# Kernel tuning notes

Hardware: AMD Instinct MI355X
Metric: run time of the kernel (lower is better)

## Reference

```python
import jax, jax.numpy as jnp
import numpy as np

MAX_ITER = 3
MIN = -1e32


def setup_inputs() -> dict:
    key = jax.random.key(0)
    k1, k2 = jax.random.split(key)
    B, L = 8, 160
    s_arc = jax.random.normal(k1, (B, L, L), dtype=jnp.float32)
    s_sib = jax.random.normal(k2, (B, L, L, L), dtype=jnp.float32)
    mask = jnp.ones((B, L), dtype=bool)
    return {"s_arc": s_arc, "s_sib": s_sib, "mask": mask}


def _lbp(s_arc, s_sib, mask):
    B, L = mask.shape
    ar = jnp.arange(L)
    ls = jnp.minimum(ar[:, None], ar[None, :])  # [L,L] min(i,j)
    rs = jnp.maximum(ar[:, None], ar[None, :])  # [L,L] max(i,j)
    mask = mask.at[:, 0].set(True)  # root always on
    # pairwise token mask, permuted to [L, L, B]
    m2 = (mask[:, :, None] & mask[:, None, :]).transpose(2, 1, 0)
    # second-order mask [head, dep, sib, B]
    mask2o = m2[:, None, :, :] & m2[:, :, None, :]
    mask2o = mask2o & (ls[:, :, None] != ar[None, None, :])[..., None]
    mask2o = mask2o & (rs[:, :, None] != ar[None, None, :])[..., None]
    s_arc_p = s_arc.transpose(2, 1, 0)  # [head, dep, B]
    s_sib_p = jnp.where(mask2o, s_sib.transpose(2, 1, 3, 0), MIN)  # [head, dep, sib, B]
    q = s_arc_p
    m_sib = jnp.zeros((L, L, L, B), dtype=s_arc.dtype)
    for _ in range(MAX_ITER):
        q = jax.nn.log_softmax(q, axis=0)  # normalize over heads
        m = q[:, :, None, :] - m_sib  # [h, d, s, B]
        m_sib = jax.nn.log_softmax(
            jnp.logaddexp(jax.nn.logsumexp(m, axis=0), m + s_sib_p).transpose(0, 2, 1, 3),
            axis=0,
        )
        q = s_arc_p + jnp.sum(m_sib * mask2o, axis=2)
    return q.transpose(2, 1, 0)  # [B, dep, head]


def reference(s_arc, s_sib, mask):
    logits = _lbp(s_arc, s_sib, mask)
    marginals = jax.nn.softmax(logits, axis=-1)
    return marginals
```

## Files before the change

kernel.cpp:

```cpp
#include <hip/hip_runtime.h>
#include <math.h>


constexpr int L = 160;
constexpr int B = 8;
constexpr int NT = 256;
constexpr int CHUNK = 32;
constexpr float INV_LN2 = 1.4426950408889634f;

#if __has_builtin(__builtin_amdgcn_exp2f)
__device__ __forceinline__ float ex2(float x) { return __builtin_amdgcn_exp2f(x); }
#else
__device__ __forceinline__ float ex2(float x) { return exp2f(x); }
#endif
#if __has_builtin(__builtin_amdgcn_logf)
__device__ __forceinline__ float lg2(float x) { return __builtin_amdgcn_logf(x); }
#else
__device__ __forceinline__ float lg2(float x) { return log2f(x); }
#endif

template <int IMM>
__device__ __forceinline__ float swz(float v) {
  return __int_as_float(__builtin_amdgcn_ds_swizzle(__float_as_int(v), IMM));
}
template <int CTRL>
__device__ __forceinline__ float dppmov(float x) {
  return __int_as_float(
      __builtin_amdgcn_update_dpp(0, __float_as_int(x), CTRL, 0xF, 0xF, true));
}
__device__ __forceinline__ void rsum64x2(float& a, float& b) {
  a += dppmov<0x121>(a); b += dppmov<0x121>(b);
  a += dppmov<0x122>(a); b += dppmov<0x122>(b);
  a += dppmov<0x124>(a); b += dppmov<0x124>(b);
  a += dppmov<0x128>(a); b += dppmov<0x128>(b);
  a += swz<0x401F>(a);   b += swz<0x401F>(b);
  a += __shfl_xor(a, 32, 64);
  b += __shfl_xor(b, 32, 64);
}
__device__ __forceinline__ float wsum(float v) {
  v += swz<0x041F>(v); v += swz<0x081F>(v); v += swz<0x101F>(v);
  v += swz<0x201F>(v); v += swz<0x401F>(v);
  v += __shfl_xor(v, 32, 64);
  return v;
}
__device__ __forceinline__ float wmax(float v) {
  v = fmaxf(v, swz<0x041F>(v)); v = fmaxf(v, swz<0x081F>(v));
  v = fmaxf(v, swz<0x101F>(v)); v = fmaxf(v, swz<0x201F>(v));
  v = fmaxf(v, swz<0x401F>(v));
  v = fmaxf(v, __shfl_xor(v, 32, 64));
  return v;
}

template <bool FIRST>
__device__ __forceinline__ void phaseAB(const float* __restrict__ s_arc,
                                        const float* __restrict__ Min, int slab,
                                        int b, int d, int t, int lane,
                                        float* qn, float4 (*qpart)[40], float* s_lse) {
  if constexpr (!FIRST) {
    if (t < 240) {
      const int h4 = t % 40, sr = t / 40;
      float ax = 0.f, ay = 0.f, az = 0.f, aw = 0.f;
#pragma unroll 4
      for (int i = 0; i < 27; ++i) {
        const int s = sr + 6 * i;
        if (s < L) {
          const float4 v = *reinterpret_cast<const float4*>(Min + slab + s * L + 4 * h4);
          ax += (s != 4 * h4 + 0 && s != d) ? v.x : 0.f;
          ay += (s != 4 * h4 + 1 && s != d) ? v.y : 0.f;
          az += (s != 4 * h4 + 2 && s != d) ? v.z : 0.f;
          aw += (s != 4 * h4 + 3 && s != d) ? v.w : 0.f;
        }
      }
      qpart[sr][h4] = make_float4(ax, ay, az, aw);
    }
    __syncthreads();
    if (t < 40) {
      float4 a = qpart[0][t];
#pragma unroll
      for (int sr = 1; sr < 6; ++sr) {
        const float4 p = qpart[sr][t];
        a.x += p.x; a.y += p.y; a.z += p.z; a.w += p.w;
      }
      const float4 sa = *reinterpret_cast<const float4*>(s_arc + (b * L + d) * L + 4 * t);
      a.x += sa.x * INV_LN2; a.y += sa.y * INV_LN2;
      a.z += sa.z * INV_LN2; a.w += sa.w * INV_LN2;
      *reinterpret_cast<float4*>(qn + 4 * t) = a;
    }
  } else {
    if (t < 40) {
      float4 sa = *reinterpret_cast<const float4*>(s_arc + (b * L + d) * L + 4 * t);
      sa.x *= INV_LN2; sa.y *= INV_LN2; sa.z *= INV_LN2; sa.w *= INV_LN2;
      *reinterpret_cast<float4*>(qn + 4 * t) = sa;
    }
  }
  __syncthreads();
  if (t < 64) {
    const int h0 = lane, h1 = lane + 64, h2 = lane + 128;
    const bool has2 = lane < 32;
    float v0 = qn[h0], v1 = qn[h1];
    float v2 = has2 ? qn[h2] : -INFINITY;
    float mx = wmax(fmaxf(fmaxf(v0, v1), v2));
    float sm = wsum(ex2(v0 - mx) + ex2(v1 - mx) + (has2 ? ex2(v2 - mx) : 0.f));
    if (lane == 0) *s_lse = mx + lg2(sm);
  }
  __syncthreads();
  if (t < L) qn[t] -= *s_lse;
  __syncthreads();
}

template <bool FIRST>
__global__ __launch_bounds__(NT) void lbp_iter(const float* __restrict__ s_arc,
                                               const float* __restrict__ s_sib,
                                               const float* __restrict__ Min,
                                               float* __restrict__ Mout) {
  const int d = blockIdx.x, b = blockIdx.y;
  const int t = threadIdx.x, lane = t & 63, w = t >> 6;

  __shared__ __align__(16) float qn[L];
  __shared__ __align__(16) float4 qpart[6][40];
  __shared__ __align__(16) float ss2[CHUNK][L];
  __shared__ float s_lse;

  const int slab = (b * L + d) * (L * L);

  phaseAB<FIRST>(s_arc, Min, slab, b, d, t, lane, qn, qpart, &s_lse);

  float q0 = 0.f, q1 = 0.f, q2 = 0.f, q3 = 0.f;
  if (lane < 40) {
    const float4 qv = *reinterpret_cast<const float4*>(qn + 4 * lane);
    q0 = qv.x; q1 = qv.y; q2 = qv.z; q3 = qv.w;
  }

  for (int c = 0; c < L / CHUNK; ++c) {
    const int s0 = c * CHUNK;
    const float* base = s_sib + slab;
    float4 sv[5];
#pragma unroll
    for (int i = 0; i < 5; ++i) {
      const int f = t + NT * i;
      const int h = f >> 3, sl4 = f & 7;
      sv[i] = *reinterpret_cast<const float4*>(base + h * L + s0 + 4 * sl4);
    }
    const int sw = s0 + w * 8;
    float4 mr[8];
    if constexpr (!FIRST) {
      if (lane < 40) {
#pragma unroll
        for (int i = 0; i < 8; ++i)
          mr[i] = *reinterpret_cast<const float4*>(Min + slab + (sw + i) * L + 4 * lane);
      }
    }
#pragma unroll
    for (int i = 0; i < 5; ++i) {
      const int f = t + NT * i;
      const int h = f >> 3, sl4 = f & 7;
      const int h4 = h >> 2, e = h & 3;
      const float* vv = reinterpret_cast<const float*>(&sv[i]);
#pragma unroll
      for (int j = 0; j < 4; ++j) {
        const int sl = 4 * sl4 + j;
        const int cc = (sl + (sl >> 3)) & 7;
        ss2[sl][4 * (h4 ^ cc) + e] = vv[j] * INV_LN2;
      }
    }
    __syncthreads();

#pragma unroll
    for (int i = 0; i < 8; ++i) {
      const int s = sw + i;
      const int sl = s - s0;
      float s1 = 0.f, s2 = 0.f, et0 = 0.f, et1 = 0.f, et2 = 0.f, et3 = 0.f;
      if (lane < 40) {
        const int cc = (sl + (sl >> 3)) & 7;
        const float4 ssv = *reinterpret_cast<const float4*>(&ss2[sl][4 * (lane ^ cc)]);
        float mm0, mm1, mm2, mm3;
        if constexpr (FIRST) {
          mm0 = q0; mm1 = q1; mm2 = q2; mm3 = q3;
        } else {
          mm0 = q0 - mr[i].x; mm1 = q1 - mr[i].y;
          mm2 = q2 - mr[i].z; mm3 = q3 - mr[i].w;
        }
        s1 = ex2(mm0) + ex2(mm1) + ex2(mm2) + ex2(mm3);
        const int hb = 4 * lane;
        et0 = (s != hb + 0 && s != d) ? ex2(mm0 + ssv.x) : 0.f;
        et1 = (s != hb + 1 && s != d) ? ex2(mm1 + ssv.y) : 0.f;
        et2 = (s != hb + 2 && s != d) ? ex2(mm2 + ssv.z) : 0.f;
        et3 = (s != hb + 3 && s != d) ? ex2(mm3 + ssv.w) : 0.f;
        s2 = et0 + et1 + et2 + et3;
      }
      rsum64x2(s1, s2);
      if (lane < 40) {
        const float nd = lg2(160.f * s1 + s2);
        float4 o;
        o.x = lg2(s1 + et0) - nd;
        o.y = lg2(s1 + et1) - nd;
        o.z = lg2(s1 + et2) - nd;
        o.w = lg2(s1 + et3) - nd;
        *reinterpret_cast<float4*>(Mout + ((b * L + s) * L + d) * L + 4 * lane) = o;
      }
    }
    __syncthreads();
  }
}

__global__ __launch_bounds__(NT) void lbp_final(const float* __restrict__ s_arc,
                                                const float* __restrict__ Min,
                                                float* __restrict__ out) {
  const int d = blockIdx.x, b = blockIdx.y;
  const int t = threadIdx.x, lane = t & 63;
  __shared__ __align__(16) float qn[L];
  __shared__ __align__(16) float4 qpart[6][40];
  __shared__ float s_lse;
  const int slab = (b * L + d) * (L * L);

  phaseAB<false>(s_arc, Min, slab, b, d, t, lane, qn, qpart, &s_lse);

  if (t < L) out[(b * L + d) * L + t] = ex2(qn[t]);
}

extern "C" void kernel_launch(void* const* d_in, const int* in_sizes, int n_in,
                              void* d_out, int out_size, void* d_ws, size_t ws_size,
                              hipStream_t stream) {
  (void)in_sizes; (void)n_in; (void)out_size; (void)ws_size;
  const float* s_arc = (const float*)d_in[0];
  const float* s_sib = (const float*)d_in[1];
  float* out = (float*)d_out;

  const size_t MELEMS = (size_t)B * L * L * L;
  float* MA = (float*)d_ws;
  float* MB = MA + MELEMS;

  dim3 grid(L, B), block(NT);
  hipLaunchKernelGGL((lbp_iter<true>), grid, block, 0, stream, s_arc, s_sib, (const float*)nullptr, MA);
  hipLaunchKernelGGL((lbp_iter<false>), grid, block, 0, stream, s_arc, s_sib, MA, MB);
  hipLaunchKernelGGL((lbp_iter<false>), grid, block, 0, stream, s_arc, s_sib, MB, MA);
  hipLaunchKernelGGL(lbp_final, grid, block, 0, stream, s_arc, MA, out);
}
```

Baseline: 430.7 us.

## Prefetch next s_sib chunk and batch wave reductions via DPP row scans

Loads the next chunk of s_sib into registers while the current chunk is being computed, and only writes it to shared memory after the compute step. This overlaps global loads with the exp/log work. The per-row wave reductions are batched four at a time using DPP row_shr and row_bcast scans, with lane 63 read back via readlane instead of swizzle and shuffle. In the first iteration it also drops the s1 sum and uses S1 = 1, on the basis that q is normalized. The trade-off is higher register pressure from holding the prefetch buffer and the batched arrays.

```diff
diff --git a/kernel.cpp b/kernel.cpp
--- a/kernel.cpp
+++ b/kernel.cpp
@@ -23,19 +23,34 @@
 __device__ __forceinline__ float swz(float v) {
   return __int_as_float(__builtin_amdgcn_ds_swizzle(__float_as_int(v), IMM));
 }
-template <int CTRL>
-__device__ __forceinline__ float dppmov(float x) {
-  return __int_as_float(
-      __builtin_amdgcn_update_dpp(0, __float_as_int(x), CTRL, 0xF, 0xF, true));
-}
-__device__ __forceinline__ void rsum64x2(float& a, float& b) {
-  a += dppmov<0x121>(a); b += dppmov<0x121>(b);
-  a += dppmov<0x122>(a); b += dppmov<0x122>(b);
-  a += dppmov<0x124>(a); b += dppmov<0x124>(b);
-  a += dppmov<0x128>(a); b += dppmov<0x128>(b);
-  a += swz<0x401F>(a);   b += swz<0x401F>(b);
-  a += __shfl_xor(a, 32, 64);
-  b += __shfl_xor(b, 32, 64);
+template <int CTRL, int RM>
+__device__ __forceinline__ float dppadd(float v) {
+  return v + __int_as_float(__builtin_amdgcn_update_dpp(
+                 0, __float_as_int(v), CTRL, RM, 0xF, true));
+}
+template <int CTRL, int RM>
+__device__ __forceinline__ void dstep2(float (&a)[4], float (&b)[4]) {
+#pragma unroll
+  for (int k = 0; k < 4; ++k) {
+    a[k] = dppadd<CTRL, RM>(a[k]);
+    b[k] = dppadd<CTRL, RM>(b[k]);
+  }
+}
+__device__ __forceinline__ void scanreduce2(float (&a)[4], float (&b)[4]) {
+  dstep2<0x111, 0xF>(a, b); dstep2<0x112, 0xF>(a, b); dstep2<0x114, 0xF>(a, b);
+  dstep2<0x118, 0xF>(a, b); dstep2<0x142, 0xA>(a, b); dstep2<0x143, 0xC>(a, b);
+}
+template <int CTRL, int RM>
+__device__ __forceinline__ void dstep1(float (&b)[4]) {
+#pragma unroll
+  for (int k = 0; k < 4; ++k) b[k] = dppadd<CTRL, RM>(b[k]);
+}
+__device__ __forceinline__ void scanreduce1(float (&b)[4]) {
+  dstep1<0x111, 0xF>(b); dstep1<0x112, 0xF>(b); dstep1<0x114, 0xF>(b);
+  dstep1<0x118, 0xF>(b); dstep1<0x142, 0xA>(b); dstep1<0x143, 0xC>(b);
+}
+__device__ __forceinline__ float bcast63(float v) {
+  return __int_as_float(__builtin_amdgcn_readlane(__float_as_int(v), 63));
 }
 __device__ __forceinline__ float wsum(float v) {
   v += swz<0x041F>(v); v += swz<0x081F>(v); v += swz<0x101F>(v);
@@ -131,15 +146,39 @@
     q0 = qv.x; q1 = qv.y; q2 = qv.z; q3 = qv.w;
   }
 
+  const float* base = s_sib + slab;
+  float4 sv[5];
+  auto stage_write = [&]() {
+#pragma unroll
+    for (int i = 0; i < 5; ++i) {
+      const int f = t + NT * i, h = f >> 3, sl4 = f & 7;
+      const int h4 = h >> 2, e = h & 3;
+      const float* vv = reinterpret_cast<const float*>(&sv[i]);
+#pragma unroll
+      for (int j = 0; j < 4; ++j) {
+        const int sl = 4 * sl4 + j;
+        const int cc = (sl + (sl >> 3)) & 7;
+        ss2[sl][4 * (h4 ^ cc) + e] = vv[j] * INV_LN2;
+      }
+    }
+  };
+
+#pragma unroll
+  for (int i = 0; i < 5; ++i) {
+    const int f = t + NT * i, h = f >> 3, sl4 = f & 7;
+    sv[i] = *reinterpret_cast<const float4*>(base + h * L + 4 * sl4);
+  }
+  stage_write();
+  __syncthreads();
+
   for (int c = 0; c < L / CHUNK; ++c) {
     const int s0 = c * CHUNK;
-    const float* base = s_sib + slab;
-    float4 sv[5];
-#pragma unroll
-    for (int i = 0; i < 5; ++i) {
-      const int f = t + NT * i;
-      const int h = f >> 3, sl4 = f & 7;
-      sv[i] = *reinterpret_cast<const float4*>(base + h * L + s0 + 4 * sl4);
+    if (c < L / CHUNK - 1) {
+#pragma unroll
+      for (int i = 0; i < 5; ++i) {
+        const int f = t + NT * i, h = f >> 3, sl4 = f & 7;
+        sv[i] = *reinterpret_cast<const float4*>(base + h * L + (s0 + CHUNK) + 4 * sl4);
+      }
     }
     const int sw = s0 + w * 8;
     float4 mr[8];
@@ -151,55 +190,54 @@
       }
     }
 #pragma unroll
-    for (int i = 0; i < 5; ++i) {
-      const int f = t + NT * i;
-      const int h = f >> 3, sl4 = f & 7;
-      const int h4 = h >> 2, e = h & 3;
-      const float* vv = reinterpret_cast<const float*>(&sv[i]);
-#pragma unroll
-      for (int j = 0; j < 4; ++j) {
-        const int sl = 4 * sl4 + j;
-        const int cc = (sl + (sl >> 3)) & 7;
-        ss2[sl][4 * (h4 ^ cc) + e] = vv[j] * INV_LN2;
+    for (int g = 0; g < 2; ++g) {
+      float p1[4], p2[4], et0[4], et1[4], et2[4], et3[4];
+#pragma unroll
+      for (int k = 0; k < 4; ++k) {
+        const int i = 4 * g + k, s = sw + i, sl = s - s0;
+        p1[k] = 0.f; p2[k] = 0.f;
+        et0[k] = 0.f; et1[k] = 0.f; et2[k] = 0.f; et3[k] = 0.f;
+        if (lane < 40) {
+          const int cc = (sl + (sl >> 3)) & 7;
+          const float4 ssv = *reinterpret_cast<const float4*>(&ss2[sl][4 * (lane ^ cc)]);
+          float mm0, mm1, mm2, mm3;
+          if constexpr (FIRST) {
+            mm0 = q0; mm1 = q1; mm2 = q2; mm3 = q3;
+          } else {
+            mm0 = q0 - mr[i].x; mm1 = q1 - mr[i].y;
+            mm2 = q2 - mr[i].z; mm3 = q3 - mr[i].w;
+            p1[k] = ex2(mm0) + ex2(mm1) + ex2(mm2) + ex2(mm3);
+          }
+          const int hb = 4 * lane;
+          et0[k] = (s != hb + 0 && s != d) ? ex2(mm0 + ssv.x) : 0.f;
+          et1[k] = (s != hb + 1 && s != d) ? ex2(mm1 + ssv.y) : 0.f;
+          et2[k] = (s != hb + 2 && s != d) ? ex2(mm2 + ssv.z) : 0.f;
+          et3[k] = (s != hb + 3 && s != d) ? ex2(mm3 + ssv.w) : 0.f;
+          p2[k] = et0[k] + et1[k] + et2[k] + et3[k];
+        }
+      }
+      if constexpr (FIRST) scanreduce1(p2); else scanreduce2(p1, p2);
+#pragma unroll
+      for (int k = 0; k < 4; ++k) {
+        const int s = sw + 4 * g + k;
+        const float S1 = FIRST ? 1.f : bcast63(p1[k]);
+        const float S2 = bcast63(p2[k]);
+        if (lane < 40) {
+          const float nd = lg2(160.f * S1 + S2);
+          float4 o;
+          o.x = lg2(S1 + et0[k]) - nd;
+          o.y = lg2(S1 + et1[k]) - nd;
+          o.z = lg2(S1 + et2[k]) - nd;
+          o.w = lg2(S1 + et3[k]) - nd;
+          *reinterpret_cast<float4*>(Mout + ((b * L + s) * L + d) * L + 4 * lane) = o;
+        }
       }
     }
     __syncthreads();
-
-#pragma unroll
-    for (int i = 0; i < 8; ++i) {
-      const int s = sw + i;
-      const int sl = s - s0;
-      float s1 = 0.f, s2 = 0.f, et0 = 0.f, et1 = 0.f, et2 = 0.f, et3 = 0.f;
-      if (lane < 40) {
-        const int cc = (sl + (sl >> 3)) & 7;
-        const float4 ssv = *reinterpret_cast<const float4*>(&ss2[sl][4 * (lane ^ cc)]);
-        float mm0, mm1, mm2, mm3;
-        if constexpr (FIRST) {
-          mm0 = q0; mm1 = q1; mm2 = q2; mm3 = q3;
-        } else {
-          mm0 = q0 - mr[i].x; mm1 = q1 - mr[i].y;
-          mm2 = q2 - mr[i].z; mm3 = q3 - mr[i].w;
-        }
-        s1 = ex2(mm0) + ex2(mm1) + ex2(mm2) + ex2(mm3);
-        const int hb = 4 * lane;
-        et0 = (s != hb + 0 && s != d) ? ex2(mm0 + ssv.x) : 0.f;
-        et1 = (s != hb + 1 && s != d) ? ex2(mm1 + ssv.y) : 0.f;
-        et2 = (s != hb + 2 && s != d) ? ex2(mm2 + ssv.z) : 0.f;
-        et3 = (s != hb + 3 && s != d) ? ex2(mm3 + ssv.w) : 0.f;
-        s2 = et0 + et1 + et2 + et3;
-      }
-      rsum64x2(s1, s2);
-      if (lane < 40) {
-        const float nd = lg2(160.f * s1 + s2);
-        float4 o;
-        o.x = lg2(s1 + et0) - nd;
-        o.y = lg2(s1 + et1) - nd;
-        o.z = lg2(s1 + et2) - nd;
-        o.w = lg2(s1 + et3) - nd;
-        *reinterpret_cast<float4*>(Mout + ((b * L + s) * L + d) * L + 4 * lane) = o;
-      }
-    }
-    __syncthreads();
+    if (c < L / CHUNK - 1) {
+      stage_write();
+      __syncthreads();
+    }
   }
 }
 
```

New measurement: 436.5 us. About the same (+1.3%).
